# Kernel optimization log

Hardware: AMD Instinct MI355X
Metric: run time of the kernel (lower is better)

## Reference

```python
import jax, jax.numpy as jnp
import numpy as np

NUM_HEADS = 16


def setup_inputs() -> dict:
    key = jax.random.key(0)
    ks = jax.random.split(key, 5)
    S, B, N, C = 4, 2, 2048, 1024
    return {
        "x_all": jax.random.normal(ks[0], (S, B, N, C), dtype=jnp.float32),
        "w_qkv": jax.random.normal(ks[1], (C, 3 * C), dtype=jnp.float32) * (C ** -0.5),
        "b_qkv": jax.random.normal(ks[2], (3 * C,), dtype=jnp.float32) * 0.02,
        "w_proj": jax.random.normal(ks[3], (C, C), dtype=jnp.float32) * (C ** -0.5),
        "b_proj": jax.random.normal(ks[4], (C,), dtype=jnp.float32) * 0.02,
    }


def reference(x_all, w_qkv, b_qkv, w_proj, b_proj):
    # x_all: [S, B, N, C] -- S = cp_dim ring shards, each rank holds [B, N, C]
    S, B, N, C = x_all.shape
    H = NUM_HEADS
    D = C // H
    scale = 1.0 / np.sqrt(D).astype(np.float32)

    # same qkv projection on every rank
    qkv = (jnp.einsum("sbnc,ce->sbne", x_all, w_qkv) + b_qkv)
    qkv = qkv.reshape(S, B, N, 3, H, D)
    # rank 0's queries: [B, H, N, D]
    q = jnp.transpose(qkv[0, :, :, 0], (0, 2, 1, 3))
    # all shards' keys/values: [S, B, H, N, D]
    k = jnp.transpose(qkv[:, :, :, 1], (0, 1, 3, 2, 4))
    v = jnp.transpose(qkv[:, :, :, 2], (0, 1, 3, 2, 4))

    # ring loop: online softmax merge across KV shards (numerically stable
    # form of the source's exp(lse)-weighted average)
    attn_out, lse = None, None
    for s in range(S):
        scores = jnp.einsum("bhnd,bhmd->bhnm", q, k[s]) * scale  # [B,H,N,N]
        new_lse = jax.nn.logsumexp(scores, axis=-1)               # [B,H,N]
        probs = jnp.exp(scores - new_lse[..., None])
        new_out = jnp.einsum("bhnm,bhmd->bhnd", probs, v[s])      # [B,H,N,D]
        if attn_out is None:
            attn_out, lse = new_out, new_lse
        else:
            m = jnp.logaddexp(lse, new_lse)
            attn_out = (attn_out * jnp.exp(lse - m)[..., None]
                        + new_out * jnp.exp(new_lse - m)[..., None])
            lse = m

    # [B,H,N,D] -> [B,N,C]
    out = jnp.transpose(attn_out, (0, 2, 1, 3)).reshape(B, N, C)
    return out @ w_proj + b_proj
```

## Files before the change

kernel.cpp:

```cpp
#include <hip/hip_runtime.h>
#include <hip/hip_bf16.h>


typedef __bf16 bf16x8 __attribute__((ext_vector_type(8)));
typedef float v4f __attribute__((ext_vector_type(4)));

#if __has_builtin(__builtin_amdgcn_exp2f)
#define EXP2F(x) __builtin_amdgcn_exp2f(x)
#else
#define EXP2F(x) exp2f(x)
#endif

__device__ __forceinline__ float bf2f(unsigned short h) {
  union { unsigned int u; float f; } a; a.u = ((unsigned int)h) << 16; return a.f;
}
__device__ __forceinline__ unsigned short f2bf(float f) {
  union { float f; unsigned int u; } a; a.f = f;
  unsigned int u = a.u;
  unsigned int r = (u + 0x7fffu + ((u >> 16) & 1u)) >> 16;
  return (unsigned short)r;
}
__device__ __forceinline__ unsigned int pack2t(float a, float b) {
  union { float f; unsigned int u; } ua, ub; ua.f = a; ub.f = b;
  return (ua.u >> 16) | (ub.u & 0xffff0000u);
}
__device__ __forceinline__ bf16x8 ldfrag16(const unsigned short* p) {
  union { uint4 u; bf16x8 v; } x; x.u = *(const uint4*)p; return x.v;
}
__device__ __forceinline__ bf16x8 ones8() {
  union { unsigned short s[8]; bf16x8 v; } x;
#pragma unroll
  for (int i = 0; i < 8; i++) x.s[i] = 0x3F80;
  return x.v;
}
__device__ __forceinline__ void gld_lds16(const unsigned short* g, unsigned short* l) {
  __builtin_amdgcn_global_load_lds((__attribute__((address_space(1))) void*)g,
                                   (__attribute__((address_space(3))) void*)l, 16, 0, 0);
}

__global__ void detect_dtype(const unsigned short* __restrict__ x, int* flag) {
  __shared__ int cnt;
  if (threadIdx.x == 0) cnt = 0;
  __syncthreads();
  int sane = 0;
#pragma unroll
  for (int j = 0; j < 4; j++) {
    unsigned short v = x[2 * (threadIdx.x + 64 * j)];
    int e = (v >> 7) & 0xFF;
    if (e >= 90 && e <= 140) sane++;
  }
  atomicAdd(&cnt, sane);
  __syncthreads();
  if (threadIdx.x == 0) *flag = (cnt > 160) ? 0 : 1;
}

__global__ void conv_to_bf16(const void* __restrict__ in, unsigned short* __restrict__ out,
                             int n4, const int* __restrict__ flag) {
  int i = blockIdx.x * blockDim.x + threadIdx.x;
  if (i >= n4) return;
  if (*flag) {
    float4 v = ((const float4*)in)[i];
    ushort4 o;
    o.x = f2bf(v.x); o.y = f2bf(v.y); o.z = f2bf(v.z); o.w = f2bf(v.w);
    ((ushort4*)out)[i] = o;
  } else {
    ((ushort4*)out)[i] = ((const ushort4*)in)[i];
  }
}

__global__ void conv_bias(const void* __restrict__ bq_in, const void* __restrict__ bp_in,
                          unsigned short* __restrict__ bq, unsigned short* __restrict__ bp,
                          const int* __restrict__ flag) {
  int i = blockIdx.x * 256 + threadIdx.x;
  const void* in = (i < 768) ? bq_in : bp_in;
  unsigned short* out = (i < 768) ? bq : bp;
  int j = (i < 768) ? i : i - 768;
  if (*flag) {
    float4 v = ((const float4*)in)[j];
    ushort4 o;
    o.x = f2bf(v.x); o.y = f2bf(v.y); o.z = f2bf(v.z); o.w = f2bf(v.w);
    ((ushort4*)out)[j] = o;
  } else {
    ((ushort4*)out)[j] = ((const ushort4*)in)[j];
  }
}

__global__ void trans_both(const void* __restrict__ wqkv, const void* __restrict__ wproj,
                           unsigned short* __restrict__ wt1, unsigned short* __restrict__ wt2,
                           const int* __restrict__ flag) {
  __shared__ unsigned short t[32][33];
  int tx = threadIdx.x, ty = threadIdx.y;
  int bx = blockIdx.x;
  const void* in; unsigned short* out; int C, c0;
  if (bx < 96) { in = wqkv; out = wt1; C = 3072; c0 = bx * 32; }
  else         { in = wproj; out = wt2; C = 1024; c0 = (bx - 96) * 32; }
  const int R = 1024;
  int r0 = blockIdx.y * 32;
  int fp = *flag;
#pragma unroll
  for (int j = 0; j < 32; j += 8) {
    unsigned short v;
    if (fp) v = f2bf(((const float*)in)[(r0 + ty + j) * C + c0 + tx]);
    else    v = ((const unsigned short*)in)[(r0 + ty + j) * C + c0 + tx];
    t[ty + j][tx] = v;
  }
  __syncthreads();
#pragma unroll
  for (int j = 0; j < 32; j += 8) out[(c0 + ty + j) * R + r0 + tx] = t[tx][ty + j];
}

template <int MODE>
__launch_bounds__(256, 3)
__global__ void gemm_bt(const unsigned short* __restrict__ A,
                        const unsigned short* __restrict__ Bt,
                        const unsigned short* __restrict__ bias,
                        void* __restrict__ Cout,
                        int K, int ldc, const int* __restrict__ flag,
                        const unsigned short* Bt2, const unsigned short* bias2,
                        void* Cout2) {
  __shared__ unsigned short As[128 * 32];
  __shared__ unsigned short Bs[128 * 32];
  int tid = threadIdx.x;
  int w = tid >> 6, lane = tid & 63, col = lane & 15, quad = lane >> 4;
  int wm = w >> 1, wn = w & 1;
  int n0 = blockIdx.x * 128;
  int m0 = blockIdx.y * 128;
  const unsigned short* Bt_ = Bt;
  const unsigned short* bias_ = bias;
  void* Cout_ = Cout;
  bool isq = false;
  if constexpr (MODE == 3) {
    if (blockIdx.y >= 128) {
      m0 = (blockIdx.y - 128) * 128;
      Bt_ = Bt2; bias_ = bias2; Cout_ = Cout2;
      isq = true;
    }
  }
  int fp = 0;
  if constexpr (MODE == 2) fp = *flag;

  v4f acc[4][4];
#pragma unroll
  for (int i = 0; i < 4; i++)
#pragma unroll
    for (int j = 0; j < 4; j++) acc[i][j] = v4f{0.f, 0.f, 0.f, 0.f};

  int ra0 = tid >> 2, cc = tid & 3;
  const unsigned short* ga0 = &A[(m0 + ra0) * K + cc * 8];
  const unsigned short* ga1 = ga0 + 64 * K;
  const unsigned short* gb0 = &Bt_[(n0 + ra0) * K + cc * 8];
  const unsigned short* gb1 = gb0 + 64 * K;
  unsigned short* lA0 = &As[(w * 16) * 32];
  unsigned short* lA1 = &As[(64 + w * 16) * 32];
  unsigned short* lB0 = &Bs[(w * 16) * 32];
  unsigned short* lB1 = &Bs[(64 + w * 16) * 32];

  int niter = K >> 5;
  for (int it = 0; it < niter; it++) {
    __syncthreads();
    gld_lds16(ga0, lA0); gld_lds16(ga1, lA1);
    gld_lds16(gb0, lB0); gld_lds16(gb1, lB1);
    ga0 += 32; ga1 += 32; gb0 += 32; gb1 += 32;
    __syncthreads();
    bf16x8 af[4], bfr[4];
#pragma unroll
    for (int mi = 0; mi < 4; mi++) af[mi] = ldfrag16(&As[(wm * 64 + mi * 16 + col) * 32 + quad * 8]);
#pragma unroll
    for (int ni = 0; ni < 4; ni++) bfr[ni] = ldfrag16(&Bs[(wn * 64 + ni * 16 + col) * 32 + quad * 8]);
#pragma unroll
    for (int mi = 0; mi < 4; mi++)
#pragma unroll
      for (int ni = 0; ni < 4; ni++)
        acc[mi][ni] = __builtin_amdgcn_mfma_f32_16x16x32_bf16(af[mi], bfr[ni], acc[mi][ni], 0, 0, 0);
  }

  float bv[4];
#pragma unroll
  for (int ni = 0; ni < 4; ni++) bv[ni] = bf2f(bias_[n0 + wn * 64 + ni * 16 + col]);

  if constexpr (MODE == 1) {
    int rgb0 = m0 + wm * 64;
    int s = rgb0 >> 12, b = (rgb0 >> 11) & 1, n = rgb0 & 2047;
    int kvg0 = s * 2048 + n;
#pragma unroll
    for (int ni = 0; ni < 4; ni++) {
      int cg = n0 + wn * 64 + ni * 16 + col;
      int h = cg >> 6, d = cg & 63;
      unsigned short* rowp = &((unsigned short*)Cout_)[((b * 16 + h) * 64 + d) * 8192 + kvg0];
      float bvn = bv[ni];
#pragma unroll
      for (int r = 0; r < 4; r++) {
        ushort2 e, o2;
        e.x = f2bf(acc[0][ni][r] + bvn);
        e.y = f2bf(acc[2][ni][r] + bvn);
        o2.x = f2bf(acc[1][ni][r] + bvn);
        o2.y = f2bf(acc[3][ni][r] + bvn);
        *(ushort2*)&rowp[2 * (quad * 4 + r)] = e;
        *(ushort2*)&rowp[32 + 2 * (quad * 4 + r)] = o2;
      }
    }
  } else {
#pragma unroll
    for (int mi = 0; mi < 4; mi++)
#pragma unroll
      for (int ni = 0; ni < 4; ni++) {
        float vals[4];
#pragma unroll
        for (int r = 0; r < 4; r++) vals[r] = acc[mi][ni][r] + bv[ni];
        if constexpr (MODE == 3) {
          if (isq) {
#pragma unroll
            for (int r = 0; r < 4; r++) vals[r] *= 0.1803368801111601f;
          }
        }
        int rgb = m0 + wm * 64 + mi * 16 + quad * 4;
        int cg  = n0 + wn * 64 + ni * 16 + col;
        if constexpr (MODE == 0 || MODE == 3) {
          unsigned short* C = (unsigned short*)Cout_;
#pragma unroll
          for (int r = 0; r < 4; r++) C[(rgb + r) * ldc + cg] = f2bf(vals[r]);
        } else {
          if (fp) {
            float* C = (float*)Cout_;
#pragma unroll
            for (int r = 0; r < 4; r++) C[(rgb + r) * ldc + cg] = vals[r];
          } else {
            unsigned short* C = (unsigned short*)Cout_;
#pragma unroll
            for (int r = 0; r < 4; r++) C[(rgb + r) * ldc + cg] = f2bf(vals[r]);
          }
        }
      }
  }
}

__launch_bounds__(512, 4)
__global__ void attn_kernel(const unsigned short* __restrict__ qbuf,
                            const unsigned short* __restrict__ kbuf,
                            const unsigned short* __restrict__ vt,
                            float* __restrict__ po,
                            float* __restrict__ lbuf) {
  __shared__ unsigned short Ks[2][64 * 64];
  __shared__ unsigned short Vs[3][64 * 64];
  int tid = threadIdx.x;
  int w = tid >> 6, lane = tid & 63, col = lane & 15, quad = lane >> 4;
  int id = blockIdx.x;
  int xcd = id & 7, slot = id >> 3;
  int qt = slot & 7, gsub = slot >> 3;
  int g = gsub * 8 + xcd;
  int bh = g >> 1, half = g & 1;
  int b = bh >> 4, h = bh & 15;
  int q0 = qt * 256;

  bf16x8 aQ[2][2];
#pragma unroll
  for (int mj = 0; mj < 2; mj++)
#pragma unroll
    for (int kk = 0; kk < 2; kk++)
      aQ[mj][kk] = ldfrag16(&qbuf[(b * 2048 + q0 + w * 32 + mj * 16 + col) * 1024 +
                                  h * 64 + kk * 32 + quad * 8]);

  int r0 = tid >> 3, c0 = tid & 7;
  const unsigned short* kp = &kbuf[((half * 2) * 4096 + b * 2048 + r0) * 1024 + h * 64 + c0 * 8];
  const unsigned short* vp = &vt[(bh * 64 + r0) * 8192 + half * 4096 + c0 * 8];
  int sdst = r0 * 64 + 8 * (c0 ^ (r0 & 7));

  const bf16x8 vone = ones8();
  v4f o[2][4];
  v4f acc_l[2] = {v4f{0.f, 0.f, 0.f, 0.f}, v4f{0.f, 0.f, 0.f, 0.f}};
#pragma unroll
  for (int mj = 0; mj < 2; mj++)
#pragma unroll
    for (int di = 0; di < 4; di++) o[mj][di] = v4f{0.f, 0.f, 0.f, 0.f};

  {
    uint4 k0 = *(const uint4*)kp, v0 = *(const uint4*)vp;
    *(uint4*)&Ks[0][sdst] = k0;
    *(uint4*)&Vs[0][sdst] = v0;
  }
  kp += 64 * 1024; vp += 64;
  uint4 pk = *(const uint4*)kp, pv = *(const uint4*)vp;
  __syncthreads();

  bf16x8 aP[2][2];
  {
    v4f sc[4][2];
#pragma unroll
    for (int ni = 0; ni < 4; ni++)
#pragma unroll
      for (int mj = 0; mj < 2; mj++) sc[ni][mj] = v4f{0.f, 0.f, 0.f, 0.f};
#pragma unroll
    for (int kk = 0; kk < 2; kk++) {
      bf16x8 aK[4];
#pragma unroll
      for (int ni = 0; ni < 4; ni++) {
        int row = ni * 16 + col;
        aK[ni] = ldfrag16(&Ks[0][row * 64 + 8 * ((kk * 4 + quad) ^ (col & 7))]);
      }
#pragma unroll
      for (int ni = 0; ni < 4; ni++)
#pragma unroll
        for (int mj = 0; mj < 2; mj++)
          sc[ni][mj] = __builtin_amdgcn_mfma_f32_16x16x32_bf16(aK[ni], aQ[mj][kk], sc[ni][mj], 0, 0, 0);
    }
#pragma unroll
    for (int ni = 0; ni < 4; ni++)
#pragma unroll
      for (int mj = 0; mj < 2; mj++)
#pragma unroll
        for (int r = 0; r < 4; r++) sc[ni][mj][r] = EXP2F(sc[ni][mj][r]);
#pragma unroll
    for (int mj = 0; mj < 2; mj++)
#pragma unroll
      for (int kk = 0; kk < 2; kk++) {
        union { unsigned int d[4]; bf16x8 v; } u;
#pragma unroll
        for (int t = 0; t < 4; t++)
          u.d[t] = pack2t(sc[kk][mj][t], sc[kk + 2][mj][t]);
        aP[mj][kk] = u.v;
      }
  }
  *(uint4*)&Ks[1][sdst] = pk;
  *(uint4*)&Vs[1][sdst] = pv;
  __syncthreads();

  const unsigned short* vprev = Vs[0];
  const unsigned short* vcur  = Vs[1];
  const unsigned short* vnext = Vs[2];

  for (int t = 1; t < 64; t++) {
    const unsigned short* kcur = Ks[t & 1];
    unsigned short* knxt = (unsigned short*)Ks[(t + 1) & 1];
    if (t < 63) {
      int kstep = (((t + 1) & 31) == 0) ? (2048 + 64) * 1024 : 64 * 1024;
      kp += kstep; vp += 64;
      pk = *(const uint4*)kp; pv = *(const uint4*)vp;
    }

    v4f sc[4][2];
#pragma unroll
    for (int ni = 0; ni < 4; ni++)
#pragma unroll
      for (int mj = 0; mj < 2; mj++) sc[ni][mj] = v4f{0.f, 0.f, 0.f, 0.f};
#pragma unroll
    for (int kk = 0; kk < 2; kk++) {
      bf16x8 aK[4];
#pragma unroll
      for (int ni = 0; ni < 4; ni++) {
        int row = ni * 16 + col;
        aK[ni] = ldfrag16(&kcur[row * 64 + 8 * ((kk * 4 + quad) ^ (col & 7))]);
      }
#pragma unroll
      for (int ni = 0; ni < 4; ni++)
#pragma unroll
        for (int mj = 0; mj < 2; mj++)
          sc[ni][mj] = __builtin_amdgcn_mfma_f32_16x16x32_bf16(aK[ni], aQ[mj][kk], sc[ni][mj], 0, 0, 0);
    }

#pragma unroll
    for (int kk = 0; kk < 2; kk++) {
#pragma unroll
      for (int mj = 0; mj < 2; mj++)
        acc_l[mj] = __builtin_amdgcn_mfma_f32_16x16x32_bf16(aP[mj][kk], vone, acc_l[mj], 0, 0, 0);
      bf16x8 bV[4];
#pragma unroll
      for (int di = 0; di < 4; di++) {
        int row = di * 16 + col;
        bV[di] = ldfrag16(&vprev[row * 64 + 8 * ((kk * 4 + quad) ^ (col & 7))]);
      }
#pragma unroll
      for (int mj = 0; mj < 2; mj++)
#pragma unroll
        for (int di = 0; di < 4; di++)
          o[mj][di] = __builtin_amdgcn_mfma_f32_16x16x32_bf16(aP[mj][kk], bV[di], o[mj][di], 0, 0, 0);
    }

#pragma unroll
    for (int ni = 0; ni < 4; ni++)
#pragma unroll
      for (int mj = 0; mj < 2; mj++)
#pragma unroll
        for (int r = 0; r < 4; r++) sc[ni][mj][r] = EXP2F(sc[ni][mj][r]);
    bf16x8 aPn[2][2];
#pragma unroll
    for (int mj = 0; mj < 2; mj++)
#pragma unroll
      for (int kk = 0; kk < 2; kk++) {
        union { unsigned int d[4]; bf16x8 v; } u;
#pragma unroll
        for (int tt = 0; tt < 4; tt++)
          u.d[tt] = pack2t(sc[kk][mj][tt], sc[kk + 2][mj][tt]);
        aPn[mj][kk] = u.v;
      }

    if (t < 63) {
      *(uint4*)&knxt[sdst] = pk;
      *(uint4*)&((unsigned short*)vnext)[sdst] = pv;
    }

    __syncthreads();

#pragma unroll
    for (int mj = 0; mj < 2; mj++)
#pragma unroll
      for (int kk = 0; kk < 2; kk++) aP[mj][kk] = aPn[mj][kk];
    const unsigned short* vt_ = vprev;
    vprev = vcur; vcur = vnext; vnext = vt_;
  }

#pragma unroll
  for (int kk = 0; kk < 2; kk++) {
#pragma unroll
    for (int mj = 0; mj < 2; mj++)
      acc_l[mj] = __builtin_amdgcn_mfma_f32_16x16x32_bf16(aP[mj][kk], vone, acc_l[mj], 0, 0, 0);
    bf16x8 bV[4];
#pragma unroll
    for (int di = 0; di < 4; di++) {
      int row = di * 16 + col;
      bV[di] = ldfrag16(&vprev[row * 64 + 8 * ((kk * 4 + quad) ^ (col & 7))]);
    }
#pragma unroll
    for (int mj = 0; mj < 2; mj++)
#pragma unroll
      for (int di = 0; di < 4; di++)
        o[mj][di] = __builtin_amdgcn_mfma_f32_16x16x32_bf16(aP[mj][kk], bV[di], o[mj][di], 0, 0, 0);
  }

  float* pb = po + half * 4194304;
#pragma unroll
  for (int mj = 0; mj < 2; mj++)
#pragma unroll
    for (int r = 0; r < 4; r++) {
      int n = q0 + w * 32 + mj * 16 + quad * 4 + r;
      if (col == 0) lbuf[half * 65536 + (b * 16 + h) * 2048 + n] = acc_l[mj][r];
#pragma unroll
      for (int di = 0; di < 4; di++) {
        int c = h * 64 + di * 16 + col;
        pb[(b * 2048 + n) * 1024 + c] = o[mj][di][r];
      }
    }
}

__global__ void merge_halves(const float* __restrict__ po, const float* __restrict__ lbuf,
                             unsigned short* __restrict__ attn) {
  int i = blockIdx.x * 256 + threadIdx.x;
  int r = i >> 8, c4 = i & 255;
  float l = lbuf[((r >> 11) * 16 + (c4 >> 4)) * 2048 + (r & 2047)] +
            lbuf[65536 + ((r >> 11) * 16 + (c4 >> 4)) * 2048 + (r & 2047)];
  float inv = 1.f / l;
  float4 a = ((const float4*)po)[i];
  float4 b = ((const float4*)po)[1048576 + i];
  ushort4 o;
  o.x = f2bf((a.x + b.x) * inv); o.y = f2bf((a.y + b.y) * inv);
  o.z = f2bf((a.z + b.z) * inv); o.w = f2bf((a.w + b.w) * inv);
  ((ushort4*)attn)[i] = o;
}

extern "C" void kernel_launch(void* const* d_in, const int* in_sizes, int n_in,
                              void* d_out, int out_size, void* d_ws, size_t ws_size,
                              hipStream_t stream) {
  const void* x      = d_in[0];
  const void* w_qkv  = d_in[1];
  const void* b_qkv  = d_in[2];
  const void* w_proj = d_in[3];
  const void* b_proj = d_in[4];

  char* ws = (char*)d_ws;
  unsigned short* xb   = (unsigned short*)(ws);
  unsigned short* kk   = (unsigned short*)(ws + 33554432);
  unsigned short* vt   = (unsigned short*)(ws + 67108864);
  unsigned short* q0b  = (unsigned short*)(ws + 100663296);
  unsigned short* attn = (unsigned short*)(ws + 109051904);
  unsigned short* wt1  = (unsigned short*)(ws + 117440512);
  unsigned short* wt2  = (unsigned short*)(ws + 123731968);
  unsigned short* bq   = (unsigned short*)(ws + 125829120);
  unsigned short* bp   = (unsigned short*)(ws + 125835264);
  int* flag            = (int*)(ws + 125837312);
  float* po   = (float*)xb;
  float* lbuf = (float*)wt1;

  detect_dtype<<<1, 64, 0, stream>>>((const unsigned short*)x, flag);

  conv_to_bf16<<<16384, 256, 0, stream>>>(x, xb, 4194304, flag);
  conv_bias<<<4, 256, 0, stream>>>(b_qkv, b_proj, bq, bp, flag);
  trans_both<<<dim3(128, 32), dim3(32, 8), 0, stream>>>(w_qkv, w_proj, wt1, wt2, flag);

  gemm_bt<3><<<dim3(8, 160), 256, 0, stream>>>(xb, wt1 + 1024 * 1024, bq + 1024, kk,
                                               1024, 1024, flag, wt1, bq, q0b);
  gemm_bt<1><<<dim3(8, 128), 256, 0, stream>>>(xb, wt1 + 2048 * 1024, bq + 2048, vt,
                                               1024, 0, flag, nullptr, nullptr, nullptr);

  attn_kernel<<<512, 512, 0, stream>>>(q0b, kk, vt, po, lbuf);
  merge_halves<<<4096, 256, 0, stream>>>(po, lbuf, attn);

  gemm_bt<2><<<dim3(8, 32), 256, 0, stream>>>(attn, wt2, bp, d_out,
                                              1024, 1024, flag, nullptr, nullptr, nullptr);
}
```

Baseline: 314.2 us.

## Merge K/Q and V projection GEMMs into one launch with XCD-aware tile mapping

Combines the K+Q and V projection GEMMs into a single 1D-grid launch, so K and V tiles that share the same A rows are interleaved. Blocks are remapped so that each XCD (block id mod 8) handles a contiguous group of M rows across all eight N tiles, which is meant to keep A tiles resident in that XCD's L2. The output projection GEMM uses the same XCD-aware mapping. This removes one kernel launch and tail effect, at the cost of extra per-block branching on the pointer and epilogue choice.

```diff
diff --git a/kernel.cpp b/kernel.cpp
--- a/kernel.cpp
+++ b/kernel.cpp
@@ -117,24 +117,36 @@
                         void* __restrict__ Cout,
                         int K, int ldc, const int* __restrict__ flag,
                         const unsigned short* Bt2, const unsigned short* bias2,
-                        void* Cout2) {
+                        void* Cout2,
+                        const unsigned short* Bt3, const unsigned short* bias3,
+                        void* Cout3) {
   __shared__ unsigned short As[128 * 32];
   __shared__ unsigned short Bs[128 * 32];
   int tid = threadIdx.x;
   int w = tid >> 6, lane = tid & 63, col = lane & 15, quad = lane >> 4;
   int wm = w >> 1, wn = w & 1;
-  int n0 = blockIdx.x * 128;
-  int m0 = blockIdx.y * 128;
   const unsigned short* Bt_ = Bt;
   const unsigned short* bias_ = bias;
   void* Cout_ = Cout;
-  bool isq = false;
-  if constexpr (MODE == 3) {
-    if (blockIdx.y >= 128) {
-      m0 = (blockIdx.y - 128) * 128;
-      Bt_ = Bt2; bias_ = bias2; Cout_ = Cout2;
-      isq = true;
-    }
+  bool isq = false, isv = false;
+  int n0, m0;
+  if constexpr (MODE == 4) {
+    int id = blockIdx.x;
+    int xcd = id & 7, t = id >> 3;
+    n0 = (t & 7) * 128;
+    int y = xcd * 36 + (t >> 3);
+    if (y < 256) {
+      m0 = (y >> 1) * 128;
+      if (y & 1) { isv = true; Bt_ = Bt3; bias_ = bias3; Cout_ = Cout3; }
+    } else {
+      m0 = (y - 256) * 128;
+      isq = true; Bt_ = Bt2; bias_ = bias2; Cout_ = Cout2;
+    }
+  } else {
+    int id = blockIdx.x;
+    int xcd = id & 7, t = id >> 3;
+    n0 = (t & 7) * 128;
+    m0 = (xcd * 4 + (t >> 3)) * 128;
   }
   int fp = 0;
   if constexpr (MODE == 2) fp = *flag;
@@ -178,7 +190,7 @@
 #pragma unroll
   for (int ni = 0; ni < 4; ni++) bv[ni] = bf2f(bias_[n0 + wn * 64 + ni * 16 + col]);
 
-  if constexpr (MODE == 1) {
+  if (MODE == 4 && isv) {
     int rgb0 = m0 + wm * 64;
     int s = rgb0 >> 12, b = (rgb0 >> 11) & 1, n = rgb0 & 2047;
     int kvg0 = s * 2048 + n;
@@ -207,7 +219,7 @@
         float vals[4];
 #pragma unroll
         for (int r = 0; r < 4; r++) vals[r] = acc[mi][ni][r] + bv[ni];
-        if constexpr (MODE == 3) {
+        if constexpr (MODE == 4) {
           if (isq) {
 #pragma unroll
             for (int r = 0; r < 4; r++) vals[r] *= 0.1803368801111601f;
@@ -215,7 +227,7 @@
         }
         int rgb = m0 + wm * 64 + mi * 16 + quad * 4;
         int cg  = n0 + wn * 64 + ni * 16 + col;
-        if constexpr (MODE == 0 || MODE == 3) {
+        if constexpr (MODE == 4) {
           unsigned short* C = (unsigned short*)Cout_;
 #pragma unroll
           for (int r = 0; r < 4; r++) C[(rgb + r) * ldc + cg] = f2bf(vals[r]);
@@ -485,14 +497,16 @@
   conv_bias<<<4, 256, 0, stream>>>(b_qkv, b_proj, bq, bp, flag);
   trans_both<<<dim3(128, 32), dim3(32, 8), 0, stream>>>(w_qkv, w_proj, wt1, wt2, flag);
 
-  gemm_bt<3><<<dim3(8, 160), 256, 0, stream>>>(xb, wt1 + 1024 * 1024, bq + 1024, kk,
-                                               1024, 1024, flag, wt1, bq, q0b);
-  gemm_bt<1><<<dim3(8, 128), 256, 0, stream>>>(xb, wt1 + 2048 * 1024, bq + 2048, vt,
-                                               1024, 0, flag, nullptr, nullptr, nullptr);
+  gemm_bt<4><<<2304, 256, 0, stream>>>(xb, wt1 + 1024 * 1024, bq + 1024, kk,
+                                       1024, 1024, flag,
+                                       wt1, bq, q0b,
+                                       wt1 + 2048 * 1024, bq + 2048, vt);
 
   attn_kernel<<<512, 512, 0, stream>>>(q0b, kk, vt, po, lbuf);
   merge_halves<<<4096, 256, 0, stream>>>(po, lbuf, attn);
 
-  gemm_bt<2><<<dim3(8, 32), 256, 0, stream>>>(attn, wt2, bp, d_out,
-                                              1024, 1024, flag, nullptr, nullptr, nullptr);
-}
+  gemm_bt<2><<<256, 256, 0, stream>>>(attn, wt2, bp, d_out,
+                                      1024, 1024, flag,
+                                      nullptr, nullptr, nullptr,
+                                      nullptr, nullptr, nullptr);
+}
```

After: 291.6 us. 7.2% less time.
